# Performance work log

Measured on AMD Instinct MI355X. Metric: run time of the kernel, lower is better.

Reference implementation:

```python
import jax, jax.numpy as jnp
import numpy as np


def masked_softmax(v, mask, axis):
    # Faithful to the torch helper (memory_efficient=False branch):
    # softmax(v * mask), re-mask, renormalize with eps.
    m = mask.astype(v.dtype)
    r = jax.nn.softmax(v * m, axis=axis)
    r = r * m
    return r / (r.sum(axis=axis, keepdims=True) + 1e-13)


def setup_inputs() -> dict:
    key = jax.random.key(0)
    ks = jax.random.split(key, 7)
    B, L1, L2, D, A = 64, 512, 512, 512, 256
    s = 0.05  # keep tanh inputs in a non-saturated range
    return {
        "seq_features1": jax.random.normal(ks[0], (B, L1, D), jnp.float32),
        "seq_features2": jax.random.normal(ks[1], (B, L2, D), jnp.float32),
        "mask1": jnp.ones((B, L1), jnp.int32),
        "mask2": jnp.ones((B, L2), jnp.int32),
        "W": jax.random.normal(ks[2], (D, D), jnp.float32) * s,
        "Wv": jax.random.normal(ks[3], (D, A), jnp.float32) * s,
        "Wq": jax.random.normal(ks[4], (D, A), jnp.float32) * s,
        "w_hv": jax.random.normal(ks[5], (A, 1), jnp.float32) * s,
        "w_hq": jax.random.normal(ks[6], (A, 1), jnp.float32) * s,
    }


def reference(seq_features1, seq_features2, mask1, mask2, W, Wv, Wq, w_hv, w_hq):
    # C: [B, L1, L2] bilinear affinity, tanh-squashed
    C = jnp.tanh(jnp.einsum('bld,de,bme->blm', seq_features1, W, seq_features2))
    s1Wv = seq_features1 @ Wv  # [B, L1, A]
    s2Wq = seq_features2 @ Wq  # [B, L2, A]
    Hv = jnp.tanh(s1Wv + C @ s2Wq)                                  # [B, L1, A]
    Hq = jnp.tanh(s2Wq + jnp.einsum('blm,bla->bma', C, s1Wv))       # [B, L2, A]
    attn_v = masked_softmax((Hv @ w_hv)[..., 0], mask1, 1)          # [B, L1]
    attn_q = masked_softmax((Hq @ w_hq)[..., 0], mask2, 1)          # [B, L2]
    v_hat = jnp.einsum('bl,bld->bd', attn_v, seq_features1)         # [B, D]
    q_hat = jnp.einsum('bm,bmd->bd', attn_q, seq_features2)         # [B, D]
    return (v_hat, q_hat)
```

## Files before the change

### kernel.cpp

```cpp
#include <hip/hip_runtime.h>

typedef _Float16 f16;
typedef _Float16 f16x8 __attribute__((ext_vector_type(8)));
typedef _Float16 f16x4 __attribute__((ext_vector_type(4)));
typedef float f32x4 __attribute__((ext_vector_type(4)));

#define BM 128
#define BN 128

__device__ __forceinline__ float fast_tanh(float x) {
    return 1.0f - 2.0f / (__expf(2.0f * x) + 1.0f);
}

__device__ __forceinline__ void ld16(const void* g, void* l) {
    __builtin_amdgcn_global_load_lds(
        (const __attribute__((address_space(1))) void*)g,
        (__attribute__((address_space(3))) void*)l, 16, 0, 0);
}

__global__ __launch_bounds__(256) void prep(
    const float* __restrict__ s1, const float* __restrict__ s2,
    f16* __restrict__ s1b, f16* __restrict__ s2b,
    const float* __restrict__ W, const float* __restrict__ Wv,
    const float* __restrict__ Wq,
    f16* __restrict__ WTb, f16* __restrict__ WvTb, f16* __restrict__ WqTb,
    float* __restrict__ logv, float* __restrict__ out)
{
    int bid = blockIdx.x, tid = threadIdx.x;
    if (bid < 32768) {
        int g = bid * 256 + tid;
        const int F = 4194304;
        const float* src = (g < F) ? s1 : s2;
        f16* dst = (g < F) ? s1b : s2b;
        int i = (g < F) ? g : g - F;
        float4 v = ((const float4*)src)[i];
        f16x4 h = {(f16)v.x, (f16)v.y, (f16)v.z, (f16)v.w};
        *(f16x4*)(dst + 4L * i) = h;
    } else if (bid < 34816) {
        int t2 = (bid - 32768) * 256 + tid;
        if (t2 < 262144) {
            int c = t2 >> 9, r = t2 & 511;
            WTb[t2] = (f16)W[r * 512 + c];
        } else if (t2 < 393216) {
            int i = t2 - 262144;
            int c = i >> 9, r = i & 511;
            WvTb[i] = (f16)Wv[r * 256 + c];
        } else {
            int i = t2 - 393216;
            int c = i >> 9, r = i & 511;
            WqTb[i] = (f16)Wq[r * 256 + c];
        }
    } else {
        int t3 = (bid - 34816) * 256 + tid;
        float4 z = {0.f, 0.f, 0.f, 0.f};
        if (t3 < 16384) ((float4*)logv)[t3] = z;
        else ((float4*)out)[t3 - 16384] = z;
    }
}

struct Job {
    const f16* A; const f16* B;
    f16* Cout; f16* CTout;
    const f16* Sadd;
    const float* wvec;
    float* logits;
    long sA, sB, sC, sCT, sS, sL;
    int lda, ldb, ldc, ldct, ldsa;
    int mode, swz, gxl, K;
};
struct JobPack { Job j[3]; int end0, end1; };

__global__ __launch_bounds__(256, 3) void gemm_multi(JobPack jp) {
    int bid = blockIdx.x;
    int ji = (bid < jp.end0) ? 0 : ((bid < jp.end1) ? 1 : 2);
    const Job J = jp.j[ji];
    int local = bid - ((ji == 0) ? 0 : ((ji == 1) ? jp.end0 : jp.end1));

    int bx, by, bz;
    if (J.swz >= 0) {
        int tg = local >> 3;
        bz = (local & 7) + 8 * (tg >> J.swz);
        int t = tg & ((1 << J.swz) - 1);
        bx = t & ((1 << J.gxl) - 1);
        by = t >> J.gxl;
    } else {
        bz = 0;
        int x = local & 7, u = local >> 3;
        bx = u >> 5;
        by = (x << 5) | (u & 31);
    }

    const f16* Ab = J.A + (long)bz * J.sA;
    const f16* Bb = J.B + (long)bz * J.sB;
    int m0 = by * BM;
    int n0 = bx * BN;
    int tid = threadIdx.x;
    int wave = tid >> 6, lane = tid & 63;
    int quad = lane >> 4, l16 = lane & 15;
    int wm = (wave >> 1) * 64, wn = (wave & 1) * 64;

    __shared__ __align__(16) char smem[32768];
    f16* T = (f16*)smem;

    f32x4 zero = {0.f, 0.f, 0.f, 0.f};
    f32x4 acc[4][4];
#pragma unroll
    for (int i = 0; i < 4; i++)
#pragma unroll
        for (int j = 0; j < 4; j++) acc[i][j] = zero;

    int lda = J.lda, ldb = J.ldb;
    auto stage = [&](int buf, int k0) {
        f16* As = (f16*)(smem + buf * 16384);
        f16* Bs = (f16*)(smem + buf * 16384 + 8192);
#pragma unroll
        for (int j = 0; j < 2; j++) {
            int rbase = wave * 32 + j * 16;
            int r = rbase + (lane >> 2);
            int sw = ((lane & 3) ^ ((r >> 1) & 3)) << 3;
            ld16(Ab + (long)(m0 + r) * lda + k0 + sw, As + rbase * 32);
            ld16(Bb + (long)(n0 + r) * ldb + k0 + sw, Bs + rbase * 32);
        }
    };

    const int NK = J.K >> 5;
    stage(0, 0);
    for (int ki = 0; ki < NK; ki++) {
        int cur = ki & 1;
        __builtin_amdgcn_s_barrier();
        asm volatile("" ::: "memory");
        if (ki + 1 < NK) {
            stage(1 - cur, (ki + 1) << 5);
            __builtin_amdgcn_s_waitcnt(0xF74);
        } else {
            __builtin_amdgcn_s_waitcnt(0xF70);
        }
        __builtin_amdgcn_s_barrier();
        asm volatile("" ::: "memory");

        const f16* As = (const f16*)(smem + cur * 16384);
        const f16* Bs = (const f16*)(smem + cur * 16384 + 8192);
        f16x8 af[4], bfr[4];
#pragma unroll
        for (int mt = 0; mt < 4; mt++) {
            int row = wm + mt * 16 + l16;
            af[mt] = *(const f16x8*)(As + row * 32 + ((quad ^ ((row >> 1) & 3)) << 3));
        }
#pragma unroll
        for (int nt = 0; nt < 4; nt++) {
            int row = wn + nt * 16 + l16;
            bfr[nt] = *(const f16x8*)(Bs + row * 32 + ((quad ^ ((row >> 1) & 3)) << 3));
        }
#pragma unroll
        for (int mt = 0; mt < 4; mt++)
#pragma unroll
            for (int nt = 0; nt < 4; nt++)
                acc[mt][nt] = __builtin_amdgcn_mfma_f32_16x16x32_f16(af[mt], bfr[nt], acc[mt][nt], 0, 0, 0);
        asm volatile("" ::: "memory");
    }

    int gmb = m0 + wm;
    int gnb = n0 + wn;

    if (J.mode == 3) {
        const f16* Sb = J.Sadd + (long)bz * J.sS;
        float* lg = J.logits + (long)bz * J.sL;
#pragma unroll
        for (int mt = 0; mt < 4; mt++) {
            int rowb = gmb + mt * 16 + quad * 4;
            float part[4] = {0.f, 0.f, 0.f, 0.f};
#pragma unroll
            for (int nt = 0; nt < 4; nt++) {
                int col = gnb + nt * 16 + l16;
                float w = J.wvec[col];
#pragma unroll
                for (int r = 0; r < 4; r++) {
                    float s = (float)Sb[(long)(rowb + r) * J.ldsa + col];
                    part[r] += fast_tanh(s + acc[mt][nt][r]) * w;
                }
            }
#pragma unroll
            for (int off = 1; off < 16; off <<= 1) {
#pragma unroll
                for (int r = 0; r < 4; r++) part[r] += __shfl_xor(part[r], off);
            }
            if (l16 == 0) {
#pragma unroll
                for (int r = 0; r < 4; r++) atomicAdd(&lg[rowb + r], part[r]);
            }
        }
        return;
    }

    f16x4 hreg[4][4];
#pragma unroll
    for (int mt = 0; mt < 4; mt++)
#pragma unroll
        for (int nt = 0; nt < 4; nt++) {
            float v0 = acc[mt][nt][0], v1 = acc[mt][nt][1];
            float v2 = acc[mt][nt][2], v3 = acc[mt][nt][3];
            if (J.mode == 1) {
                v0 = fast_tanh(v0); v1 = fast_tanh(v1);
                v2 = fast_tanh(v2); v3 = fast_tanh(v3);
            }
            f16x4 hv = {(f16)v0, (f16)v1, (f16)v2, (f16)v3};
            hreg[mt][nt] = hv;
        }

    f16* Cb = J.Cout + (long)bz * J.sC;
#pragma unroll
    for (int mt = 0; mt < 4; mt++) {
        int rowb = gmb + mt * 16 + quad * 4;
#pragma unroll
        for (int nt = 0; nt < 4; nt++) {
            int col = gnb + nt * 16 + l16;
#pragma unroll
            for (int r = 0; r < 4; r++)
                Cb[(long)(rowb + r) * J.ldc + col] = hreg[mt][nt][r];
        }
    }

    if (J.mode == 1 || J.mode == 2) {
        long bb = (J.mode == 2) ? (m0 >> 9) : bz;
        int lr0  = (J.mode == 2) ? (m0 & 511) : m0;
        f16* CTb = J.CTout + bb * J.sCT;
#pragma unroll
        for (int h = 0; h < 2; h++) {
            __syncthreads();
            if ((wave & 1) == h) {
#pragma unroll
                for (int mt = 0; mt < 4; mt++) {
                    int rloc = wm + mt * 16 + quad * 4;
#pragma unroll
                    for (int nt = 0; nt < 4; nt++) {
                        int cloc = nt * 16 + l16;
                        *(f16x4*)(T + cloc * 136 + rloc) = hreg[mt][nt];
                    }
                }
            }
            __syncthreads();
#pragma unroll
            for (int i = 0; i < 4; i++) {
                int id = tid + i * 256;
                int c = id >> 4, r8 = (id & 15) * 8;
                f16x8 v = *(const f16x8*)(T + c * 136 + r8);
                *(f16x8*)(CTb + (long)(n0 + h * 64 + c) * J.ldct + lr0 + r8) = v;
            }
        }
    }
}

__device__ __forceinline__ float block_reduce(float v, float* red, int tid, bool is_max) {
#pragma unroll
    for (int off = 32; off >= 1; off >>= 1) {
        float o = __shfl_xor(v, off);
        v = is_max ? fmaxf(v, o) : (v + o);
    }
    if ((tid & 63) == 0) red[tid >> 6] = v;
    __syncthreads();
    float t = red[0];
#pragma unroll
    for (int i = 1; i < 8; i++) t = is_max ? fmaxf(t, red[i]) : (t + red[i]);
    __syncthreads();
    return t;
}

__global__ __launch_bounds__(512) void softmax_gather(
    const float* __restrict__ logits_v, const float* __restrict__ logits_q,
    const int* __restrict__ mask1, const int* __restrict__ mask2,
    const float* __restrict__ s1f, const float* __restrict__ s2f,
    const f16* __restrict__ s1h, const f16* __restrict__ s2h, int use_h,
    float* __restrict__ out)
{
    int b = blockIdx.x;
    int which = blockIdx.y;
    int zp = blockIdx.z;
    const float* lg = (which ? logits_q : logits_v) + (long)b * 512;
    const int*   mk = (which ? mask2 : mask1) + (long)b * 512;
    float* o = out + (long)which * 64 * 512 + (long)b * 512;

    int tid = threadIdx.x;
    __shared__ float p[512];
    __shared__ float red[8];

    float m = (float)mk[tid];
    float x = lg[tid] * m;
    float mx = block_reduce(x, red, tid, true);
    float e = __expf(x - mx);
    float S1 = block_reduce(e, red, tid, false);
    float r = (e / S1) * m;
    float S2 = block_reduce(r, red, tid, false);
    p[tid] = r / (S2 + 1e-13f);
    __syncthreads();

    float acc = 0.f;
    int l0 = zp * 64;
    if (use_h) {
        const f16* S = (which ? s2h : s1h) + (long)b * 512 * 512;
#pragma unroll 8
        for (int l = l0; l < l0 + 64; l++) acc += p[l] * (float)S[(long)l * 512 + tid];
    } else {
        const float* S = (which ? s2f : s1f) + (long)b * 512 * 512;
#pragma unroll 8
        for (int l = l0; l < l0 + 64; l++) acc += p[l] * S[(long)l * 512 + tid];
    }
    atomicAdd(&o[tid], acc);
}

extern "C" void kernel_launch(void* const* d_in, const int* in_sizes, int n_in,
                              void* d_out, int out_size, void* d_ws, size_t ws_size,
                              hipStream_t stream) {
    const float* s1  = (const float*)d_in[0];
    const float* s2  = (const float*)d_in[1];
    const int* mask1 = (const int*)d_in[2];
    const int* mask2 = (const int*)d_in[3];
    const float* W   = (const float*)d_in[4];
    const float* Wv  = (const float*)d_in[5];
    const float* Wq  = (const float*)d_in[6];
    const float* whv = (const float*)d_in[7];
    const float* whq = (const float*)d_in[8];
    float* out = (float*)d_out;

    const long Bn = 64, L = 512, D = 512, Aa = 256;
    char* ws = (char*)d_ws;
    size_t off = 0;
    auto alloc = [&](size_t bytes) -> char* {
        char* p = ws + off;
        off += (bytes + 255) & ~(size_t)255;
        return p;
    };
    f16* s1b   = (f16*)alloc(Bn * L * D * 2);
    f16* s2b   = (f16*)alloc(Bn * L * D * 2);
    f16* s1W   = (f16*)alloc(Bn * L * D * 2);
    f16* Cb    = (f16*)alloc(Bn * L * L * 2);
    f16* s1Wv  = (f16*)alloc(Bn * L * Aa * 2);
    f16* s1WvT = (f16*)alloc(Bn * L * Aa * 2);
    f16* s2Wq  = (f16*)alloc(Bn * L * Aa * 2);
    f16* s2WqT = (f16*)alloc(Bn * L * Aa * 2);
    f16* WTb   = (f16*)alloc(D * D * 2);
    f16* WvTb  = (f16*)alloc(D * Aa * 2);
    f16* WqTb  = (f16*)alloc(D * Aa * 2);
    float* logv = (float*)alloc(2 * Bn * L * 4);
    float* logq = logv + Bn * L;
    size_t base_off = off;
    f16* CTded = (f16*)alloc(Bn * L * L * 2);
    if (ws_size < base_off) return;
    int use_ded = (ws_size >= off) ? 1 : 0;
    f16* CTb = use_ded ? CTded : s1b;

    prep<<<dim3(34944), 256, 0, stream>>>(s1, s2, s1b, s2b, W, Wv, Wq,
                                          WTb, WvTb, WqTb, logv, out);

    Job z0{};

    {
        JobPack p{};
        Job& a = p.j[0];
        a.A = s1b; a.B = WTb; a.Cout = s1W;
        a.lda = 512; a.ldb = 512; a.ldc = 512; a.K = 512;
        a.mode = 0; a.swz = -2; a.gxl = 2;
        Job& b = p.j[1];
        b.A = s1b; b.B = WvTb; b.Cout = s1Wv; b.CTout = s1WvT;
        b.lda = 512; b.ldb = 512; b.ldc = 256; b.ldct = 512; b.sCT = L * Aa;
        b.K = 512; b.mode = 2; b.swz = -2; b.gxl = 1;
        Job& c = p.j[2];
        c.A = s2b; c.B = WqTb; c.Cout = s2Wq; c.CTout = s2WqT;
        c.lda = 512; c.ldb = 512; c.ldc = 256; c.ldct = 512; c.sCT = L * Aa;
        c.K = 512; c.mode = 2; c.swz = -2; c.gxl = 1;
        p.end0 = 1024; p.end1 = 1536;
        gemm_multi<<<dim3(2048), 256, 0, stream>>>(p);
    }

    {
        JobPack p{};
        Job& a = p.j[0];
        a.A = s1W; a.B = s2b; a.Cout = Cb; a.CTout = CTb;
        a.lda = 512; a.ldb = 512; a.ldc = 512; a.ldct = 512;
        a.sA = L * D; a.sB = L * D; a.sC = L * L; a.sCT = L * L;
        a.K = 512; a.mode = 1; a.swz = 4; a.gxl = 2;
        p.j[1] = z0; p.j[2] = z0;
        p.end0 = 1024; p.end1 = 1024;
        gemm_multi<<<dim3(1024), 256, 0, stream>>>(p);
    }

    {
        JobPack p{};
        Job& a = p.j[0];
        a.A = Cb; a.B = s2WqT; a.Sadd = s1Wv; a.wvec = whv; a.logits = logv;
        a.lda = 512; a.ldb = 512; a.ldsa = 256;
        a.sA = L * L; a.sB = Aa * L; a.sS = L * Aa; a.sL = 512;
        a.K = 512; a.mode = 3; a.swz = 3; a.gxl = 1;
        Job& b = p.j[1];
        b.A = CTb; b.B = s1WvT; b.Sadd = s2Wq; b.wvec = whq; b.logits = logq;
        b.lda = 512; b.ldb = 512; b.ldsa = 256;
        b.sA = L * L; b.sB = Aa * L; b.sS = L * Aa; b.sL = 512;
        b.K = 512; b.mode = 3; b.swz = 3; b.gxl = 1;
        p.j[2] = z0;
        p.end0 = 512; p.end1 = 1024;
        gemm_multi<<<dim3(1024), 256, 0, stream>>>(p);
    }

    softmax_gather<<<dim3((int)Bn, 2, 8), 512, 0, stream>>>(
        logv, logq, mask1, mask2, s1, s2, s1b, s2b, use_ded, out);
}
```

Before: 300.6 us.

## Fuse fp32-to-fp16 input conversion into first GEMM A-operand load

Removes the separate prep pass that converted seq_features1/2 to fp16. The first projection GEMM now loads fp32 A rows into registers, converts them, and writes them into swizzled LDS while B is still fetched by DMA. The bx==0 blocks of the s2 job also write the fp16 copy of s2 that the bilinear GEMM needs. The softmax gather now always reads fp32 features, and C-transpose always gets its own buffer. This saves a full read/write pass over both inputs, at the cost of register-staged A loads with less overlap, and the fp32 A tile is re-read by every column block.

Measured after the change: 328.8 us. +9.4%, slower.

```diff
diff --git a/kernel.cpp b/kernel.cpp
--- a/kernel.cpp
+++ b/kernel.cpp
@@ -19,25 +19,14 @@
 }
 
 __global__ __launch_bounds__(256) void prep(
-    const float* __restrict__ s1, const float* __restrict__ s2,
-    f16* __restrict__ s1b, f16* __restrict__ s2b,
     const float* __restrict__ W, const float* __restrict__ Wv,
     const float* __restrict__ Wq,
     f16* __restrict__ WTb, f16* __restrict__ WvTb, f16* __restrict__ WqTb,
     float* __restrict__ logv, float* __restrict__ out)
 {
     int bid = blockIdx.x, tid = threadIdx.x;
-    if (bid < 32768) {
-        int g = bid * 256 + tid;
-        const int F = 4194304;
-        const float* src = (g < F) ? s1 : s2;
-        f16* dst = (g < F) ? s1b : s2b;
-        int i = (g < F) ? g : g - F;
-        float4 v = ((const float4*)src)[i];
-        f16x4 h = {(f16)v.x, (f16)v.y, (f16)v.z, (f16)v.w};
-        *(f16x4*)(dst + 4L * i) = h;
-    } else if (bid < 34816) {
-        int t2 = (bid - 32768) * 256 + tid;
+    if (bid < 2048) {
+        int t2 = bid * 256 + tid;
         if (t2 < 262144) {
             int c = t2 >> 9, r = t2 & 511;
             WTb[t2] = (f16)W[r * 512 + c];
@@ -51,7 +40,7 @@
             WqTb[i] = (f16)Wq[r * 256 + c];
         }
     } else {
-        int t3 = (bid - 34816) * 256 + tid;
+        int t3 = (bid - 2048) * 256 + tid;
         float4 z = {0.f, 0.f, 0.f, 0.f};
         if (t3 < 16384) ((float4*)logv)[t3] = z;
         else ((float4*)out)[t3 - 16384] = z;
@@ -60,6 +49,8 @@
 
 struct Job {
     const f16* A; const f16* B;
+    const float* A32;
+    f16* Aout;
     f16* Cout; f16* CTout;
     const f16* Sadd;
     const float* wvec;
@@ -70,7 +61,8 @@
 };
 struct JobPack { Job j[3]; int end0, end1; };
 
-__global__ __launch_bounds__(256, 3) void gemm_multi(JobPack jp) {
+template <int STG>
+__device__ __forceinline__ void gemm_core(const JobPack& jp) {
     int bid = blockIdx.x;
     int ji = (bid < jp.end0) ? 0 : ((bid < jp.end1) ? 1 : 2);
     const Job J = jp.j[ji];
@@ -109,54 +101,124 @@
 #pragma unroll
         for (int j = 0; j < 4; j++) acc[i][j] = zero;
 
+    const int NK = J.K >> 5;
     int lda = J.lda, ldb = J.ldb;
-    auto stage = [&](int buf, int k0) {
-        f16* As = (f16*)(smem + buf * 16384);
-        f16* Bs = (f16*)(smem + buf * 16384 + 8192);
-#pragma unroll
-        for (int j = 0; j < 2; j++) {
-            int rbase = wave * 32 + j * 16;
-            int r = rbase + (lane >> 2);
-            int sw = ((lane & 3) ^ ((r >> 1) & 3)) << 3;
-            ld16(Ab + (long)(m0 + r) * lda + k0 + sw, As + rbase * 32);
-            ld16(Bb + (long)(n0 + r) * ldb + k0 + sw, Bs + rbase * 32);
-        }
-    };
-
-    const int NK = J.K >> 5;
-    stage(0, 0);
-    for (int ki = 0; ki < NK; ki++) {
-        int cur = ki & 1;
-        __builtin_amdgcn_s_barrier();
-        asm volatile("" ::: "memory");
-        if (ki + 1 < NK) {
-            stage(1 - cur, (ki + 1) << 5);
-            __builtin_amdgcn_s_waitcnt(0xF74);
-        } else {
-            __builtin_amdgcn_s_waitcnt(0xF70);
-        }
-        __builtin_amdgcn_s_barrier();
-        asm volatile("" ::: "memory");
-
-        const f16* As = (const f16*)(smem + cur * 16384);
-        const f16* Bs = (const f16*)(smem + cur * 16384 + 8192);
-        f16x8 af[4], bfr[4];
-#pragma unroll
-        for (int mt = 0; mt < 4; mt++) {
-            int row = wm + mt * 16 + l16;
-            af[mt] = *(const f16x8*)(As + row * 32 + ((quad ^ ((row >> 1) & 3)) << 3));
-        }
-#pragma unroll
-        for (int nt = 0; nt < 4; nt++) {
-            int row = wn + nt * 16 + l16;
-            bfr[nt] = *(const f16x8*)(Bs + row * 32 + ((quad ^ ((row >> 1) & 3)) << 3));
-        }
-#pragma unroll
-        for (int mt = 0; mt < 4; mt++)
-#pragma unroll
-            for (int nt = 0; nt < 4; nt++)
-                acc[mt][nt] = __builtin_amdgcn_mfma_f32_16x16x32_f16(af[mt], bfr[nt], acc[mt][nt], 0, 0, 0);
-        asm volatile("" ::: "memory");
+
+    if (STG == 0) {
+        auto stage = [&](int buf, int k0) {
+            f16* As = (f16*)(smem + buf * 16384);
+            f16* Bs = (f16*)(smem + buf * 16384 + 8192);
+#pragma unroll
+            for (int j = 0; j < 2; j++) {
+                int rbase = wave * 32 + j * 16;
+                int r = rbase + (lane >> 2);
+                int sw = ((lane & 3) ^ ((r >> 1) & 3)) << 3;
+                ld16(Ab + (long)(m0 + r) * lda + k0 + sw, As + rbase * 32);
+                ld16(Bb + (long)(n0 + r) * ldb + k0 + sw, Bs + rbase * 32);
+            }
+        };
+        stage(0, 0);
+        for (int ki = 0; ki < NK; ki++) {
+            int cur = ki & 1;
+            __builtin_amdgcn_s_barrier();
+            asm volatile("" ::: "memory");
+            if (ki + 1 < NK) {
+                stage(1 - cur, (ki + 1) << 5);
+                __builtin_amdgcn_s_waitcnt(0xF74);
+            } else {
+                __builtin_amdgcn_s_waitcnt(0xF70);
+            }
+            __builtin_amdgcn_s_barrier();
+            asm volatile("" ::: "memory");
+
+            const f16* As = (const f16*)(smem + cur * 16384);
+            const f16* Bs = (const f16*)(smem + cur * 16384 + 8192);
+            f16x8 af[4], bfr[4];
+#pragma unroll
+            for (int mt = 0; mt < 4; mt++) {
+                int row = wm + mt * 16 + l16;
+                af[mt] = *(const f16x8*)(As + row * 32 + ((quad ^ ((row >> 1) & 3)) << 3));
+            }
+#pragma unroll
+            for (int nt = 0; nt < 4; nt++) {
+                int row = wn + nt * 16 + l16;
+                bfr[nt] = *(const f16x8*)(Bs + row * 32 + ((quad ^ ((row >> 1) & 3)) << 3));
+            }
+#pragma unroll
+            for (int mt = 0; mt < 4; mt++)
+#pragma unroll
+                for (int nt = 0; nt < 4; nt++)
+                    acc[mt][nt] = __builtin_amdgcn_mfma_f32_16x16x32_f16(af[mt], bfr[nt], acc[mt][nt], 0, 0, 0);
+            asm volatile("" ::: "memory");
+        }
+    } else {
+        const float* Fb = J.A32 + (long)bz * J.sA;
+        int fr = lane >> 3;
+        int fc = (lane & 7) * 4;
+        int fq = (lane & 7) >> 1;
+        int foff = (lane & 1) * 4;
+        float4 pf[4];
+        auto loadf = [&](int k0) {
+#pragma unroll
+            for (int i = 0; i < 4; i++)
+                pf[i] = *(const float4*)(Fb + (long)(m0 + wave * 32 + i * 8 + fr) * lda + k0 + fc);
+        };
+        auto dmab = [&](int buf, int k0) {
+            f16* Bs = (f16*)(smem + buf * 16384 + 8192);
+#pragma unroll
+            for (int j = 0; j < 2; j++) {
+                int rbase = wave * 32 + j * 16;
+                int r = rbase + (lane >> 2);
+                int sw = ((lane & 3) ^ ((r >> 1) & 3)) << 3;
+                ld16(Bb + (long)(n0 + r) * ldb + k0 + sw, Bs + rbase * 32);
+            }
+        };
+        auto writef = [&](int buf, int k0) {
+            f16* As = (f16*)(smem + buf * 16384);
+#pragma unroll
+            for (int i = 0; i < 4; i++) {
+                int r = wave * 32 + i * 8 + fr;
+                int qp = fq ^ ((r >> 1) & 3);
+                f16x4 h = {(f16)pf[i].x, (f16)pf[i].y, (f16)pf[i].z, (f16)pf[i].w};
+                *(f16x4*)(As + r * 32 + qp * 8 + foff) = h;
+                if (J.Aout != nullptr && bx == 0)
+                    *(f16x4*)(J.Aout + (long)(m0 + r) * lda + k0 + fc) = h;
+            }
+        };
+
+        dmab(0, 0);
+        loadf(0);
+        for (int ki = 0; ki < NK; ki++) {
+            int cur = ki & 1;
+            __builtin_amdgcn_s_barrier();
+            asm volatile("" ::: "memory");
+            if (ki + 1 < NK) dmab(1 - cur, (ki + 1) << 5);
+            writef(cur, ki << 5);
+            if (ki + 1 < NK) loadf((ki + 1) << 5);
+            __builtin_amdgcn_s_waitcnt(0xC07F);
+            __builtin_amdgcn_s_barrier();
+            asm volatile("" ::: "memory");
+
+            const f16* As = (const f16*)(smem + cur * 16384);
+            const f16* Bs = (const f16*)(smem + cur * 16384 + 8192);
+            f16x8 af[4], bfr[4];
+#pragma unroll
+            for (int mt = 0; mt < 4; mt++) {
+                int row = wm + mt * 16 + l16;
+                af[mt] = *(const f16x8*)(As + row * 32 + ((quad ^ ((row >> 1) & 3)) << 3));
+            }
+#pragma unroll
+            for (int nt = 0; nt < 4; nt++) {
+                int row = wn + nt * 16 + l16;
+                bfr[nt] = *(const f16x8*)(Bs + row * 32 + ((quad ^ ((row >> 1) & 3)) << 3));
+            }
+#pragma unroll
+            for (int mt = 0; mt < 4; mt++)
+#pragma unroll
+                for (int nt = 0; nt < 4; nt++)
+                    acc[mt][nt] = __builtin_amdgcn_mfma_f32_16x16x32_f16(af[mt], bfr[nt], acc[mt][nt], 0, 0, 0);
+            asm volatile("" ::: "memory");
+        }
     }
 
     int gmb = m0 + wm;
@@ -250,6 +312,9 @@
     }
 }
 
+__global__ __launch_bounds__(256, 3) void gemm_dma(JobPack jp)  { gemm_core<0>(jp); }
+__global__ __launch_bounds__(256, 3) void gemm_af32(JobPack jp) { gemm_core<1>(jp); }
+
 __device__ __forceinline__ float block_reduce(float v, float* red, int tid, bool is_max) {
 #pragma unroll
     for (int off = 32; off >= 1; off >>= 1) {
@@ -269,7 +334,6 @@
     const float* __restrict__ logits_v, const float* __restrict__ logits_q,
     const int* __restrict__ mask1, const int* __restrict__ mask2,
     const float* __restrict__ s1f, const float* __restrict__ s2f,
-    const f16* __restrict__ s1h, const f16* __restrict__ s2h, int use_h,
     float* __restrict__ out)
 {
     int b = blockIdx.x;
@@ -277,6 +341,7 @@
     int zp = blockIdx.z;
     const float* lg = (which ? logits_q : logits_v) + (long)b * 512;
     const int*   mk = (which ? mask2 : mask1) + (long)b * 512;
+    const float* S  = (which ? s2f : s1f) + (long)b * 512 * 512;
     float* o = out + (long)which * 64 * 512 + (long)b * 512;
 
     int tid = threadIdx.x;
@@ -295,15 +360,8 @@
 
     float acc = 0.f;
     int l0 = zp * 64;
-    if (use_h) {
-        const f16* S = (which ? s2h : s1h) + (long)b * 512 * 512;
 #pragma unroll 8
-        for (int l = l0; l < l0 + 64; l++) acc += p[l] * (float)S[(long)l * 512 + tid];
-    } else {
-        const float* S = (which ? s2f : s1f) + (long)b * 512 * 512;
-#pragma unroll 8
-        for (int l = l0; l < l0 + 64; l++) acc += p[l] * S[(long)l * 512 + tid];
-    }
+    for (int l = l0; l < l0 + 64; l++) acc += p[l] * S[(long)l * 512 + tid];
     atomicAdd(&o[tid], acc);
 }
 
@@ -329,10 +387,10 @@
         off += (bytes + 255) & ~(size_t)255;
         return p;
     };
-    f16* s1b   = (f16*)alloc(Bn * L * D * 2);
+    f16* s1W   = (f16*)alloc(Bn * L * D * 2);
     f16* s2b   = (f16*)alloc(Bn * L * D * 2);
-    f16* s1W   = (f16*)alloc(Bn * L * D * 2);
     f16* Cb    = (f16*)alloc(Bn * L * L * 2);
+    f16* CTb   = (f16*)alloc(Bn * L * L * 2);
     f16* s1Wv  = (f16*)alloc(Bn * L * Aa * 2);
     f16* s1WvT = (f16*)alloc(Bn * L * Aa * 2);
     f16* s2Wq  = (f16*)alloc(Bn * L * Aa * 2);
@@ -342,33 +400,28 @@
     f16* WqTb  = (f16*)alloc(D * Aa * 2);
     float* logv = (float*)alloc(2 * Bn * L * 4);
     float* logq = logv + Bn * L;
-    size_t base_off = off;
-    f16* CTded = (f16*)alloc(Bn * L * L * 2);
-    if (ws_size < base_off) return;
-    int use_ded = (ws_size >= off) ? 1 : 0;
-    f16* CTb = use_ded ? CTded : s1b;
-
-    prep<<<dim3(34944), 256, 0, stream>>>(s1, s2, s1b, s2b, W, Wv, Wq,
-                                          WTb, WvTb, WqTb, logv, out);
+    if (ws_size < off) return;
+
+    prep<<<dim3(2176), 256, 0, stream>>>(W, Wv, Wq, WTb, WvTb, WqTb, logv, out);
 
     Job z0{};
 
     {
         JobPack p{};
         Job& a = p.j[0];
-        a.A = s1b; a.B = WTb; a.Cout = s1W;
+        a.A32 = s1; a.B = WTb; a.Cout = s1W;
         a.lda = 512; a.ldb = 512; a.ldc = 512; a.K = 512;
         a.mode = 0; a.swz = -2; a.gxl = 2;
         Job& b = p.j[1];
-        b.A = s1b; b.B = WvTb; b.Cout = s1Wv; b.CTout = s1WvT;
+        b.A32 = s1; b.B = WvTb; b.Cout = s1Wv; b.CTout = s1WvT;
         b.lda = 512; b.ldb = 512; b.ldc = 256; b.ldct = 512; b.sCT = L * Aa;
         b.K = 512; b.mode = 2; b.swz = -2; b.gxl = 1;
         Job& c = p.j[2];
-        c.A = s2b; c.B = WqTb; c.Cout = s2Wq; c.CTout = s2WqT;
+        c.A32 = s2; c.B = WqTb; c.Cout = s2Wq; c.CTout = s2WqT; c.Aout = s2b;
         c.lda = 512; c.ldb = 512; c.ldc = 256; c.ldct = 512; c.sCT = L * Aa;
         c.K = 512; c.mode = 2; c.swz = -2; c.gxl = 1;
         p.end0 = 1024; p.end1 = 1536;
-        gemm_multi<<<dim3(2048), 256, 0, stream>>>(p);
+        gemm_af32<<<dim3(2048), 256, 0, stream>>>(p);
     }
 
     {
@@ -380,7 +433,7 @@
         a.K = 512; a.mode = 1; a.swz = 4; a.gxl = 2;
         p.j[1] = z0; p.j[2] = z0;
         p.end0 = 1024; p.end1 = 1024;
-        gemm_multi<<<dim3(1024), 256, 0, stream>>>(p);
+        gemm_dma<<<dim3(1024), 256, 0, stream>>>(p);
     }
 
     {
@@ -397,9 +450,9 @@
         b.K = 512; b.mode = 3; b.swz = 3; b.gxl = 1;
         p.j[2] = z0;
         p.end0 = 512; p.end1 = 1024;
-        gemm_multi<<<dim3(1024), 256, 0, stream>>>(p);
+        gemm_dma<<<dim3(1024), 256, 0, stream>>>(p);
     }
 
     softmax_gather<<<dim3((int)Bn, 2, 8), 512, 0, stream>>>(
-        logv, logq, mask1, mask2, s1, s2, s1b, s2b, use_ded, out);
-}
+        logv, logq, mask1, mask2, s1, s2, out);
+}
```

## Fuse all stages into one persistent kernel with grid-wide barriers

Applied to the files above, without the earlier changes.

Replaces the five separate launches (prep, three GEMM passes, softmax-gather) with one persistent kernel of 512 blocks that loops over each stage's work items and separates stages with an atomic-counter grid barrier. The aim is to remove inter-kernel launch gaps and drain/fill tails. The softmax-gather stage is rewritten for 256 threads, each handling two elements. The risks are that occupancy is capped at 2 blocks per CU by launch bounds, the grid barrier spins, and correctness depends on all 512 blocks being co-resident.

After: 708.8 us. 136% more time.

```diff
diff --git a/kernel.cpp b/kernel.cpp
--- a/kernel.cpp
+++ b/kernel.cpp
@@ -16,46 +16,6 @@
     __builtin_amdgcn_global_load_lds(
         (const __attribute__((address_space(1))) void*)g,
         (__attribute__((address_space(3))) void*)l, 16, 0, 0);
-}
-
-__global__ __launch_bounds__(256) void prep(
-    const float* __restrict__ s1, const float* __restrict__ s2,
-    f16* __restrict__ s1b, f16* __restrict__ s2b,
-    const float* __restrict__ W, const float* __restrict__ Wv,
-    const float* __restrict__ Wq,
-    f16* __restrict__ WTb, f16* __restrict__ WvTb, f16* __restrict__ WqTb,
-    float* __restrict__ logv, float* __restrict__ out)
-{
-    int bid = blockIdx.x, tid = threadIdx.x;
-    if (bid < 32768) {
-        int g = bid * 256 + tid;
-        const int F = 4194304;
-        const float* src = (g < F) ? s1 : s2;
-        f16* dst = (g < F) ? s1b : s2b;
-        int i = (g < F) ? g : g - F;
-        float4 v = ((const float4*)src)[i];
-        f16x4 h = {(f16)v.x, (f16)v.y, (f16)v.z, (f16)v.w};
-        *(f16x4*)(dst + 4L * i) = h;
-    } else if (bid < 34816) {
-        int t2 = (bid - 32768) * 256 + tid;
-        if (t2 < 262144) {
-            int c = t2 >> 9, r = t2 & 511;
-            WTb[t2] = (f16)W[r * 512 + c];
-        } else if (t2 < 393216) {
-            int i = t2 - 262144;
-            int c = i >> 9, r = i & 511;
-            WvTb[i] = (f16)Wv[r * 256 + c];
-        } else {
-            int i = t2 - 393216;
-            int c = i >> 9, r = i & 511;
-            WqTb[i] = (f16)Wq[r * 256 + c];
-        }
-    } else {
-        int t3 = (bid - 34816) * 256 + tid;
-        float4 z = {0.f, 0.f, 0.f, 0.f};
-        if (t3 < 16384) ((float4*)logv)[t3] = z;
-        else ((float4*)out)[t3 - 16384] = z;
-    }
 }
 
 struct Job {
@@ -70,8 +30,65 @@
 };
 struct JobPack { Job j[3]; int end0, end1; };
 
-__global__ __launch_bounds__(256, 3) void gemm_multi(JobPack jp) {
-    int bid = blockIdx.x;
+struct MegaArgs {
+    JobPack pA, p2, p4;
+    const float *s1, *s2, *W, *Wv, *Wq;
+    f16 *s1b, *s2b, *WTb, *WvTb, *WqTb;
+    float *logv, *logq, *out;
+    const int *m1, *m2;
+    const f16 *s1h, *s2h;
+    const float *s1f, *s2f;
+    const float *whv, *whq;
+    int use_h;
+    unsigned int* cnt;
+};
+
+__device__ __forceinline__ void gsync(unsigned int* cnt, unsigned int target) {
+    __syncthreads();
+    if (threadIdx.x == 0) {
+        __threadfence();
+        __hip_atomic_fetch_add(cnt, 1u, __ATOMIC_ACQ_REL, __HIP_MEMORY_SCOPE_AGENT);
+        while (__hip_atomic_load(cnt, __ATOMIC_ACQUIRE, __HIP_MEMORY_SCOPE_AGENT) < target)
+            __builtin_amdgcn_s_sleep(8);
+        __threadfence();
+    }
+    __syncthreads();
+}
+
+__device__ __forceinline__ void prep_job(const MegaArgs& a, int bid) {
+    int tid = threadIdx.x;
+    if (bid < 32768) {
+        int g = bid * 256 + tid;
+        const int F = 4194304;
+        const float* src = (g < F) ? a.s1 : a.s2;
+        f16* dst = (g < F) ? a.s1b : a.s2b;
+        int i = (g < F) ? g : g - F;
+        float4 v = ((const float4*)src)[i];
+        f16x4 h = {(f16)v.x, (f16)v.y, (f16)v.z, (f16)v.w};
+        *(f16x4*)(dst + 4L * i) = h;
+    } else if (bid < 34816) {
+        int t2 = (bid - 32768) * 256 + tid;
+        if (t2 < 262144) {
+            int c = t2 >> 9, r = t2 & 511;
+            a.WTb[t2] = (f16)a.W[r * 512 + c];
+        } else if (t2 < 393216) {
+            int i = t2 - 262144;
+            int c = i >> 9, r = i & 511;
+            a.WvTb[i] = (f16)a.Wv[r * 256 + c];
+        } else {
+            int i = t2 - 393216;
+            int c = i >> 9, r = i & 511;
+            a.WqTb[i] = (f16)a.Wq[r * 256 + c];
+        }
+    } else {
+        int t3 = (bid - 34816) * 256 + tid;
+        float4 z = {0.f, 0.f, 0.f, 0.f};
+        if (t3 < 16384) ((float4*)a.logv)[t3] = z;
+        else ((float4*)a.out)[t3 - 16384] = z;
+    }
+}
+
+__device__ __forceinline__ void gemm_job(const JobPack& jp, int bid, char* smem) {
     int ji = (bid < jp.end0) ? 0 : ((bid < jp.end1) ? 1 : 2);
     const Job J = jp.j[ji];
     int local = bid - ((ji == 0) ? 0 : ((ji == 1) ? jp.end0 : jp.end1));
@@ -99,7 +116,6 @@
     int quad = lane >> 4, l16 = lane & 15;
     int wm = (wave >> 1) * 64, wn = (wave & 1) * 64;
 
-    __shared__ __align__(16) char smem[32768];
     f16* T = (f16*)smem;
 
     f32x4 zero = {0.f, 0.f, 0.f, 0.f};
@@ -189,68 +205,69 @@
                 for (int r = 0; r < 4; r++) atomicAdd(&lg[rowb + r], part[r]);
             }
         }
-        return;
-    }
-
-    f16x4 hreg[4][4];
-#pragma unroll
-    for (int mt = 0; mt < 4; mt++)
-#pragma unroll
-        for (int nt = 0; nt < 4; nt++) {
-            float v0 = acc[mt][nt][0], v1 = acc[mt][nt][1];
-            float v2 = acc[mt][nt][2], v3 = acc[mt][nt][3];
-            if (J.mode == 1) {
-                v0 = fast_tanh(v0); v1 = fast_tanh(v1);
-                v2 = fast_tanh(v2); v3 = fast_tanh(v3);
-            }
-            f16x4 hv = {(f16)v0, (f16)v1, (f16)v2, (f16)v3};
-            hreg[mt][nt] = hv;
-        }
-
-    f16* Cb = J.Cout + (long)bz * J.sC;
-#pragma unroll
-    for (int mt = 0; mt < 4; mt++) {
-        int rowb = gmb + mt * 16 + quad * 4;
-#pragma unroll
-        for (int nt = 0; nt < 4; nt++) {
-            int col = gnb + nt * 16 + l16;
-#pragma unroll
-            for (int r = 0; r < 4; r++)
-                Cb[(long)(rowb + r) * J.ldc + col] = hreg[mt][nt][r];
-        }
-    }
-
-    if (J.mode == 1 || J.mode == 2) {
-        long bb = (J.mode == 2) ? (m0 >> 9) : bz;
-        int lr0  = (J.mode == 2) ? (m0 & 511) : m0;
-        f16* CTb = J.CTout + bb * J.sCT;
-#pragma unroll
-        for (int h = 0; h < 2; h++) {
-            __syncthreads();
-            if ((wave & 1) == h) {
-#pragma unroll
-                for (int mt = 0; mt < 4; mt++) {
-                    int rloc = wm + mt * 16 + quad * 4;
-#pragma unroll
-                    for (int nt = 0; nt < 4; nt++) {
-                        int cloc = nt * 16 + l16;
-                        *(f16x4*)(T + cloc * 136 + rloc) = hreg[mt][nt];
+    } else {
+        f16x4 hreg[4][4];
+#pragma unroll
+        for (int mt = 0; mt < 4; mt++)
+#pragma unroll
+            for (int nt = 0; nt < 4; nt++) {
+                float v0 = acc[mt][nt][0], v1 = acc[mt][nt][1];
+                float v2 = acc[mt][nt][2], v3 = acc[mt][nt][3];
+                if (J.mode == 1) {
+                    v0 = fast_tanh(v0); v1 = fast_tanh(v1);
+                    v2 = fast_tanh(v2); v3 = fast_tanh(v3);
+                }
+                f16x4 hv = {(f16)v0, (f16)v1, (f16)v2, (f16)v3};
+                hreg[mt][nt] = hv;
+            }
+
+        f16* Cb = J.Cout + (long)bz * J.sC;
+#pragma unroll
+        for (int mt = 0; mt < 4; mt++) {
+            int rowb = gmb + mt * 16 + quad * 4;
+#pragma unroll
+            for (int nt = 0; nt < 4; nt++) {
+                int col = gnb + nt * 16 + l16;
+#pragma unroll
+                for (int r = 0; r < 4; r++)
+                    Cb[(long)(rowb + r) * J.ldc + col] = hreg[mt][nt][r];
+            }
+        }
+
+        if (J.mode == 1 || J.mode == 2) {
+            long bb = (J.mode == 2) ? (m0 >> 9) : bz;
+            int lr0  = (J.mode == 2) ? (m0 & 511) : m0;
+            f16* CTb = J.CTout + bb * J.sCT;
+#pragma unroll
+            for (int h = 0; h < 2; h++) {
+                __syncthreads();
+                if ((wave & 1) == h) {
+#pragma unroll
+                    for (int mt = 0; mt < 4; mt++) {
+                        int rloc = wm + mt * 16 + quad * 4;
+#pragma unroll
+                        for (int nt = 0; nt < 4; nt++) {
+                            int cloc = nt * 16 + l16;
+                            *(f16x4*)(T + cloc * 136 + rloc) = hreg[mt][nt];
+                        }
                     }
                 }
-            }
-            __syncthreads();
-#pragma unroll
-            for (int i = 0; i < 4; i++) {
-                int id = tid + i * 256;
-                int c = id >> 4, r8 = (id & 15) * 8;
-                f16x8 v = *(const f16x8*)(T + c * 136 + r8);
-                *(f16x8*)(CTb + (long)(n0 + h * 64 + c) * J.ldct + lr0 + r8) = v;
-            }
-        }
-    }
-}
-
-__device__ __forceinline__ float block_reduce(float v, float* red, int tid, bool is_max) {
+                __syncthreads();
+#pragma unroll
+                for (int i = 0; i < 4; i++) {
+                    int id = tid + i * 256;
+                    int c = id >> 4, r8 = (id & 15) * 8;
+                    f16x8 v = *(const f16x8*)(T + c * 136 + r8);
+                    *(f16x8*)(CTb + (long)(n0 + h * 64 + c) * J.ldct + lr0 + r8) = v;
+                }
+            }
+        }
+    }
+    __syncthreads();
+}
+
+__device__ __forceinline__ float red256(float v, float* red, bool is_max) {
+    int tid = threadIdx.x;
 #pragma unroll
     for (int off = 32; off >= 1; off >>= 1) {
         float o = __shfl_xor(v, off);
@@ -258,53 +275,68 @@
     }
     if ((tid & 63) == 0) red[tid >> 6] = v;
     __syncthreads();
-    float t = red[0];
-#pragma unroll
-    for (int i = 1; i < 8; i++) t = is_max ? fmaxf(t, red[i]) : (t + red[i]);
+    float t = is_max ? fmaxf(fmaxf(red[0], red[1]), fmaxf(red[2], red[3]))
+                     : (red[0] + red[1] + red[2] + red[3]);
     __syncthreads();
     return t;
 }
 
-__global__ __launch_bounds__(512) void softmax_gather(
-    const float* __restrict__ logits_v, const float* __restrict__ logits_q,
-    const int* __restrict__ mask1, const int* __restrict__ mask2,
-    const float* __restrict__ s1f, const float* __restrict__ s2f,
-    const f16* __restrict__ s1h, const f16* __restrict__ s2h, int use_h,
-    float* __restrict__ out)
-{
-    int b = blockIdx.x;
-    int which = blockIdx.y;
-    int zp = blockIdx.z;
-    const float* lg = (which ? logits_q : logits_v) + (long)b * 512;
-    const int*   mk = (which ? mask2 : mask1) + (long)b * 512;
-    float* o = out + (long)which * 64 * 512 + (long)b * 512;
-
+__device__ __forceinline__ void gather_job(const MegaArgs& a, int v, char* smem) {
+    float* p = (float*)smem;
+    float* red = (float*)(smem + 2048);
+    int b = v >> 4, which = (v >> 3) & 1, zp = v & 7;
+    const float* lg = (which ? a.logq : a.logv) + (long)b * 512;
+    const int* mk = (which ? a.m2 : a.m1) + (long)b * 512;
+    float* o = a.out + (long)which * 64 * 512 + (long)b * 512;
     int tid = threadIdx.x;
-    __shared__ float p[512];
-    __shared__ float red[8];
-
-    float m = (float)mk[tid];
-    float x = lg[tid] * m;
-    float mx = block_reduce(x, red, tid, true);
-    float e = __expf(x - mx);
-    float S1 = block_reduce(e, red, tid, false);
-    float r = (e / S1) * m;
-    float S2 = block_reduce(r, red, tid, false);
-    p[tid] = r / (S2 + 1e-13f);
-    __syncthreads();
-
-    float acc = 0.f;
+    __syncthreads();
+    float m0 = (float)mk[tid], m1f = (float)mk[tid + 256];
+    float l0v = __hip_atomic_load(&lg[tid], __ATOMIC_RELAXED, __HIP_MEMORY_SCOPE_AGENT);
+    float l1v = __hip_atomic_load(&lg[tid + 256], __ATOMIC_RELAXED, __HIP_MEMORY_SCOPE_AGENT);
+    float x0 = l0v * m0, x1 = l1v * m1f;
+    float mx = red256(fmaxf(x0, x1), red, true);
+    float e0 = __expf(x0 - mx), e1 = __expf(x1 - mx);
+    float S1 = red256(e0 + e1, red, false);
+    float r0 = (e0 / S1) * m0, r1 = (e1 / S1) * m1f;
+    float S2 = red256(r0 + r1, red, false);
+    p[tid] = r0 / (S2 + 1e-13f);
+    p[tid + 256] = r1 / (S2 + 1e-13f);
+    __syncthreads();
+    float a0 = 0.f, a1 = 0.f;
     int l0 = zp * 64;
-    if (use_h) {
-        const f16* S = (which ? s2h : s1h) + (long)b * 512 * 512;
-#pragma unroll 8
-        for (int l = l0; l < l0 + 64; l++) acc += p[l] * (float)S[(long)l * 512 + tid];
+    if (a.use_h) {
+        const f16* S = (which ? a.s2h : a.s1h) + (long)b * 262144;
+#pragma unroll 4
+        for (int l = l0; l < l0 + 64; l++) {
+            float pl = p[l];
+            a0 += pl * (float)S[(long)l * 512 + tid];
+            a1 += pl * (float)S[(long)l * 512 + tid + 256];
+        }
     } else {
-        const float* S = (which ? s2f : s1f) + (long)b * 512 * 512;
-#pragma unroll 8
-        for (int l = l0; l < l0 + 64; l++) acc += p[l] * S[(long)l * 512 + tid];
-    }
-    atomicAdd(&o[tid], acc);
+        const float* S = (which ? a.s2f : a.s1f) + (long)b * 262144;
+#pragma unroll 4
+        for (int l = l0; l < l0 + 64; l++) {
+            float pl = p[l];
+            a0 += pl * S[(long)l * 512 + tid];
+            a1 += pl * S[(long)l * 512 + tid + 256];
+        }
+    }
+    atomicAdd(&o[tid], a0);
+    atomicAdd(&o[tid + 256], a1);
+}
+
+__global__ __launch_bounds__(256, 2) void mega(MegaArgs a) {
+    __shared__ __align__(16) char smem[32768];
+    const int G = gridDim.x;
+    for (int v = blockIdx.x; v < 34944; v += G) prep_job(a, v);
+    gsync(a.cnt, 1u * G);
+    for (int v = blockIdx.x; v < 2048; v += G) gemm_job(a.pA, v, smem);
+    gsync(a.cnt, 2u * G);
+    for (int v = blockIdx.x; v < 1024; v += G) gemm_job(a.p2, v, smem);
+    gsync(a.cnt, 3u * G);
+    for (int v = blockIdx.x; v < 1024; v += G) gemm_job(a.p4, v, smem);
+    gsync(a.cnt, 4u * G);
+    for (int v = blockIdx.x; v < 1024; v += G) gather_job(a, v, smem);
 }
 
 extern "C" void kernel_launch(void* const* d_in, const int* in_sizes, int n_in,
@@ -342,64 +374,60 @@
     f16* WqTb  = (f16*)alloc(D * Aa * 2);
     float* logv = (float*)alloc(2 * Bn * L * 4);
     float* logq = logv + Bn * L;
+    unsigned int* cnt = (unsigned int*)alloc(256);
     size_t base_off = off;
     f16* CTded = (f16*)alloc(Bn * L * L * 2);
     if (ws_size < base_off) return;
     int use_ded = (ws_size >= off) ? 1 : 0;
     f16* CTb = use_ded ? CTded : s1b;
 
-    prep<<<dim3(34944), 256, 0, stream>>>(s1, s2, s1b, s2b, W, Wv, Wq,
-                                          WTb, WvTb, WqTb, logv, out);
-
-    Job z0{};
-
+    hipMemsetAsync(cnt, 0, 4, stream);
+
+    MegaArgs a{};
     {
-        JobPack p{};
-        Job& a = p.j[0];
-        a.A = s1b; a.B = WTb; a.Cout = s1W;
-        a.lda = 512; a.ldb = 512; a.ldc = 512; a.K = 512;
-        a.mode = 0; a.swz = -2; a.gxl = 2;
-        Job& b = p.j[1];
-        b.A = s1b; b.B = WvTb; b.Cout = s1Wv; b.CTout = s1WvT;
-        b.lda = 512; b.ldb = 512; b.ldc = 256; b.ldct = 512; b.sCT = L * Aa;
-        b.K = 512; b.mode = 2; b.swz = -2; b.gxl = 1;
-        Job& c = p.j[2];
-        c.A = s2b; c.B = WqTb; c.Cout = s2Wq; c.CTout = s2WqT;
-        c.lda = 512; c.ldb = 512; c.ldc = 256; c.ldct = 512; c.sCT = L * Aa;
-        c.K = 512; c.mode = 2; c.swz = -2; c.gxl = 1;
-        p.end0 = 1024; p.end1 = 1536;
-        gemm_multi<<<dim3(2048), 256, 0, stream>>>(p);
-    }
-
+        Job& j0 = a.pA.j[0];
+        j0.A = s1b; j0.B = WTb; j0.Cout = s1W;
+        j0.lda = 512; j0.ldb = 512; j0.ldc = 512; j0.K = 512;
+        j0.mode = 0; j0.swz = -2; j0.gxl = 2;
+        Job& j1 = a.pA.j[1];
+        j1.A = s1b; j1.B = WvTb; j1.Cout = s1Wv; j1.CTout = s1WvT;
+        j1.lda = 512; j1.ldb = 512; j1.ldc = 256; j1.ldct = 512; j1.sCT = L * Aa;
+        j1.K = 512; j1.mode = 2; j1.swz = -2; j1.gxl = 1;
+        Job& j2 = a.pA.j[2];
+        j2.A = s2b; j2.B = WqTb; j2.Cout = s2Wq; j2.CTout = s2WqT;
+        j2.lda = 512; j2.ldb = 512; j2.ldc = 256; j2.ldct = 512; j2.sCT = L * Aa;
+        j2.K = 512; j2.mode = 2; j2.swz = -2; j2.gxl = 1;
+        a.pA.end0 = 1024; a.pA.end1 = 1536;
+    }
     {
-        JobPack p{};
-        Job& a = p.j[0];
-        a.A = s1W; a.B = s2b; a.Cout = Cb; a.CTout = CTb;
-        a.lda = 512; a.ldb = 512; a.ldc = 512; a.ldct = 512;
-        a.sA = L * D; a.sB = L * D; a.sC = L * L; a.sCT = L * L;
-        a.K = 512; a.mode = 1; a.swz = 4; a.gxl = 2;
-        p.j[1] = z0; p.j[2] = z0;
-        p.end0 = 1024; p.end1 = 1024;
-        gemm_multi<<<dim3(1024), 256, 0, stream>>>(p);
-    }
-
+        Job& j0 = a.p2.j[0];
+        j0.A = s1W; j0.B = s2b; j0.Cout = Cb; j0.CTout = CTb;
+        j0.lda = 512; j0.ldb = 512; j0.ldc = 512; j0.ldct = 512;
+        j0.sA = L * D; j0.sB = L * D; j0.sC = L * L; j0.sCT = L * L;
+        j0.K = 512; j0.mode = 1; j0.swz = 4; j0.gxl = 2;
+        a.p2.end0 = 1024; a.p2.end1 = 1024;
+    }
     {
-        JobPack p{};
-        Job& a = p.j[0];
-        a.A = Cb; a.B = s2WqT; a.Sadd = s1Wv; a.wvec = whv; a.logits = logv;
-        a.lda = 512; a.ldb = 512; a.ldsa = 256;
-        a.sA = L * L; a.sB = Aa * L; a.sS = L * Aa; a.sL = 512;
-        a.K = 512; a.mode = 3; a.swz = 3; a.gxl = 1;
-        Job& b = p.j[1];
-        b.A = CTb; b.B = s1WvT; b.Sadd = s2Wq; b.wvec = whq; b.logits = logq;
-        b.lda = 512; b.ldb = 512; b.ldsa = 256;
-        b.sA = L * L; b.sB = Aa * L; b.sS = L * Aa; b.sL = 512;
-        b.K = 512; b.mode = 3; b.swz = 3; b.gxl = 1;
-        p.j[2] = z0;
-        p.end0 = 512; p.end1 = 1024;
-        gemm_multi<<<dim3(1024), 256, 0, stream>>>(p);
-    }
-
-    softmax_gather<<<dim3((int)Bn, 2, 8), 512, 0, stream>>>(
-        logv, logq, mask1, mask2, s1, s2, s1b, s2b, use_ded, out);
-}
+        Job& j0 = a.p4.j[0];
+        j0.A = Cb; j0.B = s2WqT; j0.Sadd = s1Wv; j0.wvec = whv; j0.logits = logv;
+        j0.lda = 512; j0.ldb = 512; j0.ldsa = 256;
+        j0.sA = L * L; j0.sB = Aa * L; j0.sS = L * Aa; j0.sL = 512;
+        j0.K = 512; j0.mode = 3; j0.swz = 3; j0.gxl = 1;
+        Job& j1 = a.p4.j[1];
+        j1.A = CTb; j1.B = s1WvT; j1.Sadd = s2Wq; j1.wvec = whq; j1.logits = logq;
+        j1.lda = 512; j1.ldb = 512; j1.ldsa = 256;
+        j1.sA = L * L; j1.sB = Aa * L; j1.sS = L * Aa; j1.sL = 512;
+        j1.K = 512; j1.mode = 3; j1.swz = 3; j1.gxl = 1;
+        a.p4.end0 = 512; a.p4.end1 = 1024;
+    }
+    a.s1 = s1; a.s2 = s2; a.W = W; a.Wv = Wv; a.Wq = Wq;
+    a.s1b = s1b; a.s2b = s2b; a.WTb = WTb; a.WvTb = WvTb; a.WqTb = WqTb;
+    a.logv = logv; a.logq = logq; a.out = out;
+    a.m1 = mask1; a.m2 = mask2;
+    a.s1h = s1b; a.s2h = s2b; a.s1f = s1; a.s2f = s2;
+    a.whv = whv; a.whq = whq;
+    a.use_h = use_ded;
+    a.cnt = cnt;
+
+    mega<<<dim3(512), dim3(256), 0, stream>>>(a);
+}
```
